# Optimization experiments

Hardware: AMD Instinct MI355X
Metric: run time of the kernel (lower is better)

The kernel has to match this reference:

```python
import math
import jax, jax.numpy as jnp
import numpy as np

B, T, D_MODEL, H = 2, 2048, 1024, 16
D_HEAD = D_MODEL // H
EPS = 1e-9


def setup_inputs() -> dict:
    key = jax.random.key(0)
    ks = jax.random.split(key, 5)
    std = 1.0 / math.sqrt(D_MODEL)
    return {
        "x": jax.random.normal(ks[0], (B, T, D_MODEL), dtype=jnp.float32),
        "Wq": jax.random.normal(ks[1], (D_MODEL, D_MODEL), dtype=jnp.float32) * std,
        "Wk": jax.random.normal(ks[2], (D_MODEL, D_MODEL), dtype=jnp.float32) * std,
        "Wv": jax.random.normal(ks[3], (D_MODEL, D_MODEL), dtype=jnp.float32) * std,
        "Wo": jax.random.normal(ks[4], (D_MODEL, D_MODEL), dtype=jnp.float32) * std,
    }


def _attention(x, Wq, Wk, Wv, Wo):
    b, t, d = x.shape
    # projections (nn.Linear without bias: y = x @ W^T)
    q = (x @ Wq.T).reshape(b, t, H, D_HEAD).transpose(0, 2, 1, 3)  # (B,H,T,dh)
    k = (x @ Wk.T).reshape(b, t, H, D_HEAD).transpose(0, 2, 1, 3)
    v = (x @ Wv.T).reshape(b, t, H, D_HEAD).transpose(0, 2, 1, 3)
    scale = 1.0 / math.sqrt(D_HEAD)
    scores = jnp.einsum("bhqd,bhkd->bhqk", q, k) * scale  # (B,H,T,T)
    causal = jnp.tril(jnp.ones((t, t), dtype=bool))
    scores = jnp.where(causal[None, None], scores, -jnp.inf)
    # stable softmax with +eps in denominator (matches online-softmax accumulation)
    m = jnp.max(scores, axis=-1, keepdims=True)
    e = jnp.exp(scores - m)
    l = jnp.sum(e, axis=-1, keepdims=True)
    attn_out = jnp.einsum("bhqk,bhkd->bhqd", e, v) / (l + EPS)
    out = attn_out.transpose(0, 2, 1, 3).reshape(b, t, d)
    return out @ Wo.T


def reference(x, Wq, Wk, Wv, Wo):
    return _attention(x, Wq, Wk, Wv, Wo)
```

## Files before the change

kernel.cpp:

```cpp
#include <hip/hip_runtime.h>


typedef __attribute__((ext_vector_type(8))) short bf16x8;
typedef __attribute__((ext_vector_type(4))) short short4v;
typedef __attribute__((ext_vector_type(4))) float f32x4;

#define T_SEQ 2048
#define D_MODEL 1024
#define NHEAD 16
#define DHEAD 64

__device__ inline short f2bf(float f) {
    unsigned u = __float_as_uint(f);
    u += 0x7fffu + ((u >> 16) & 1u);
    return (short)(u >> 16);
}

__device__ inline f32x4 mfma16(bf16x8 a, bf16x8 b, f32x4 c) {
    return __builtin_amdgcn_mfma_f32_16x16x32_bf16(a, b, c, 0, 0, 0);
}

__device__ inline void gld_lds16(const short* g, short* l) {
    __builtin_amdgcn_global_load_lds(
        (const __attribute__((address_space(1))) void*)g,
        (__attribute__((address_space(3))) void*)l, 16, 0, 0);
}

__global__ __launch_bounds__(256) void cast_kernel(const float* __restrict__ s,
                                                   short* __restrict__ d, int n) {
    int i = (blockIdx.x * 256 + threadIdx.x) * 4;
    if (i >= n) return;
    float4 v = *(const float4*)(s + i);
    short4v o = { f2bf(v.x), f2bf(v.y), f2bf(v.z), f2bf(v.w) };
    *(short4v*)(d + i) = o;
}

__global__ __launch_bounds__(256) void cast4_kernel(const float* __restrict__ s0,
                                                    const float* __restrict__ s1,
                                                    const float* __restrict__ s2,
                                                    const float* __restrict__ s3,
                                                    short* __restrict__ d) {
    const float* s = (blockIdx.y == 0) ? s0 : (blockIdx.y == 1) ? s1
                   : (blockIdx.y == 2) ? s2 : s3;
    int i = (blockIdx.x * 256 + threadIdx.x) * 4;
    float4 v = *(const float4*)(s + i);
    short4v o = { f2bf(v.x), f2bf(v.y), f2bf(v.z), f2bf(v.w) };
    *(short4v*)(d + blockIdx.y * 1048576 + i) = o;
}

template <int MODE>
__global__ __launch_bounds__(256, 2) void gemm128(const short* __restrict__ A,
                                                  const short* __restrict__ B,
                                                  void* __restrict__ C0,
                                                  void* __restrict__ C1,
                                                  void* __restrict__ C2,
                                                  int M, int N, int K) {
    __shared__ short As[4096];
    __shared__ short Bs[4096];

    const int tid = threadIdx.x;
    const int wave = tid >> 6, lane = tid & 63;
    const int g = lane >> 4, ln = lane & 15;
    const int mh = wave & 1, nh = wave >> 1;
    const int m_base = blockIdx.x * 128;
    const int n_base = blockIdx.y * 128;

    const int srow = tid >> 2;
    const int sinner = (tid & 3) * 8;
    const short* Ag = A + (long)(m_base + srow) * K + sinner;
    const short* Bg = B + (long)(n_base + srow) * K + sinner;
    const long r64 = 64 * (long)K;

    f32x4 acc[4][4];
#pragma unroll
    for (int i = 0; i < 4; i++)
#pragma unroll
        for (int j = 0; j < 4; j++) acc[i][j] = (f32x4){0.f, 0.f, 0.f, 0.f};

    for (int k0 = 0; k0 < K; k0 += 32) {
        gld_lds16(Ag + k0, As + tid * 8);
        gld_lds16(Ag + r64 + k0, As + 2048 + tid * 8);
        gld_lds16(Bg + k0, Bs + tid * 8);
        gld_lds16(Bg + r64 + k0, Bs + 2048 + tid * 8);
        __syncthreads();

        bf16x8 a[4], b[4];
#pragma unroll
        for (int mf = 0; mf < 4; mf++)
            a[mf] = *(const bf16x8*)(As + (mh * 64 + mf * 16 + ln) * 32 + g * 8);
#pragma unroll
        for (int nf = 0; nf < 4; nf++)
            b[nf] = *(const bf16x8*)(Bs + (nh * 64 + nf * 16 + ln) * 32 + g * 8);
#pragma unroll
        for (int mf = 0; mf < 4; mf++)
#pragma unroll
            for (int nf = 0; nf < 4; nf++)
                acc[mf][nf] = mfma16(a[mf], b[nf], acc[mf][nf]);
        __syncthreads();
    }

    if (MODE == 2) {
#pragma unroll
        for (int mf = 0; mf < 4; mf++)
#pragma unroll
            for (int nf = 0; nf < 4; nf++)
#pragma unroll
                for (int r = 0; r < 4; r++) {
                    int row = m_base + mh * 64 + mf * 16 + g * 4 + r;
                    int col = n_base + nh * 64 + nf * 16 + ln;
                    ((float*)C0)[(long)row * N + col] = acc[mf][nf][r];
                }
    } else {
        const int mat = n_base >> 10;
        if (mat < 2) {
            short* dst = (short*)(mat == 0 ? C0 : C1);
#pragma unroll
            for (int mf = 0; mf < 4; mf++)
#pragma unroll
                for (int nf = 0; nf < 4; nf++)
#pragma unroll
                    for (int r = 0; r < 4; r++) {
                        int row = m_base + mh * 64 + mf * 16 + g * 4 + r;
                        int cc = (n_base & 1023) + nh * 64 + nf * 16 + ln;
                        int b_ = row >> 11, t = row & 2047;
                        int h = cc >> 6, d = cc & 63;
                        dst[(((long)(b_ * NHEAD + h) * T_SEQ + t) << 6) + d] =
                            f2bf(acc[mf][nf][r]);
                    }
        } else {
            short* dst = (short*)C2;
#pragma unroll
            for (int mf = 0; mf < 4; mf++)
#pragma unroll
                for (int nf = 0; nf < 4; nf++) {
                    short4v pk = { f2bf(acc[mf][nf][0]), f2bf(acc[mf][nf][1]),
                                   f2bf(acc[mf][nf][2]), f2bf(acc[mf][nf][3]) };
                    int cc = (n_base & 1023) + nh * 64 + nf * 16 + ln;
                    int row0 = m_base + mh * 64 + mf * 16 + g * 4;
                    int b_ = row0 >> 11, t = row0 & 2047;
                    *(short4v*)(&dst[((long)(b_ * 1024 + cc) << 11) + t]) = pk;
                }
        }
    }
}

__global__ __launch_bounds__(512, 4) void flash_attn(const short* __restrict__ Q,
                                                     const short* __restrict__ Kx,
                                                     const short* __restrict__ Vt,
                                                     short* __restrict__ O) {
    __shared__ short Ks[2][4096];
    __shared__ short Vs[2][4096];
    __shared__ short ldsP[8][16][72];

    const int tid = threadIdx.x;
    const int wv = tid >> 6, lane = tid & 63;
    const int g = lane >> 4, ln = lane & 15;
    const int id = blockIdx.x;
    const int qx = 15 - (id >> 5);
    const int bh = id & 31;

    const short* Kp = Kx + (long)bh * (T_SEQ * DHEAD);
    const short* Vp = Vt + (long)bh * (DHEAD * T_SEQ);

    const int sch = tid >> 8;
    const int sr = (tid >> 2) & 63;
    const int si = (tid & 3) * 8;
    const int offK = sr * 64 + sch * 32 + si;
    const long offV = (long)sr * T_SEQ + sch * 32 + si;
    const int ldst = tid * 8;

    const float sc = 0.125f * 1.44269504089f;
    const int nt = 2 * qx + 2;
    const int qrow0 = qx * 128 + wv * 16;
    const int rl = wv * 16 + g * 4;

    const short* Qp = Q + ((long)bh * T_SEQ + qrow0) * DHEAD;
    bf16x8 qf0 = *(const bf16x8*)(Qp + ln * 64 + 8 * g);
    bf16x8 qf1 = *(const bf16x8*)(Qp + ln * 64 + 32 + 8 * g);

    f32x4 o[4];
#pragma unroll
    for (int nf = 0; nf < 4; nf++) o[nf] = (f32x4){0.f, 0.f, 0.f, 0.f};
    float li[4] = {0.f, 0.f, 0.f, 0.f};

    gld_lds16(Kp + offK, &Ks[0][ldst]);
    gld_lds16(Vp + offV, &Vs[0][ldst]);

    int buf = 0;
    for (int i = 0; i < nt; i++) {
        __syncthreads();
        if (i + 1 < nt) {
            gld_lds16(Kp + (i + 1) * 4096 + offK, &Ks[buf ^ 1][ldst]);
            gld_lds16(Vp + offV + (i + 1) * 64, &Vs[buf ^ 1][ldst]);
        }

        f32x4 s[4];
#pragma unroll
        for (int j = 0; j < 4; j++) {
            bf16x8 k0 = *(const bf16x8*)(&Ks[buf][(j * 16 + ln) * 32 + 8 * g]);
            bf16x8 k1 = *(const bf16x8*)(&Ks[buf][2048 + (j * 16 + ln) * 32 + 8 * g]);
            s[j] = mfma16(qf0, k0, (f32x4){0.f, 0.f, 0.f, 0.f});
            s[j] = mfma16(qf1, k1, s[j]);
        }

        if (i >= 2 * qx) {
            const int off = (i - 2 * qx) * 64;
#pragma unroll
            for (int j = 0; j < 4; j++) {
                int kl = off + 16 * j + ln;
#pragma unroll
                for (int r = 0; r < 4; r++)
                    if (kl > rl + r) s[j][r] = -INFINITY;
            }
        }

#pragma unroll
        for (int r = 0; r < 4; r++) {
            float e0 = __builtin_amdgcn_exp2f(s[0][r] * sc);
            float e1 = __builtin_amdgcn_exp2f(s[1][r] * sc);
            float e2 = __builtin_amdgcn_exp2f(s[2][r] * sc);
            float e3 = __builtin_amdgcn_exp2f(s[3][r] * sc);
            li[r] += (e0 + e1) + (e2 + e3);
            ldsP[wv][g * 4 + r][ln] = f2bf(e0);
            ldsP[wv][g * 4 + r][16 + ln] = f2bf(e1);
            ldsP[wv][g * 4 + r][32 + ln] = f2bf(e2);
            ldsP[wv][g * 4 + r][48 + ln] = f2bf(e3);
        }

        asm volatile("s_waitcnt lgkmcnt(0)" ::: "memory");
        bf16x8 pa0 = *(const bf16x8*)(&ldsP[wv][ln][8 * g]);
        bf16x8 pa1 = *(const bf16x8*)(&ldsP[wv][ln][32 + 8 * g]);

#pragma unroll
        for (int nf = 0; nf < 4; nf++) {
            bf16x8 v0 = *(const bf16x8*)(&Vs[buf][(nf * 16 + ln) * 32 + 8 * g]);
            bf16x8 v1 = *(const bf16x8*)(&Vs[buf][2048 + (nf * 16 + ln) * 32 + 8 * g]);
            o[nf] = mfma16(pa0, v0, o[nf]);
            o[nf] = mfma16(pa1, v1, o[nf]);
        }
        buf ^= 1;
    }

#pragma unroll
    for (int r = 0; r < 4; r++) {
        float l = li[r];
        l += __shfl_xor(l, 1);
        l += __shfl_xor(l, 2);
        l += __shfl_xor(l, 4);
        l += __shfl_xor(l, 8);
        li[r] = l;
    }
    const int b = bh >> 4, h = bh & 15;
#pragma unroll
    for (int nf = 0; nf < 4; nf++) {
#pragma unroll
        for (int r = 0; r < 4; r++) {
            int rr = qrow0 + g * 4 + r;
            float v = o[nf][r] / (li[r] + 1e-9f);
            O[((long)(b * T_SEQ + rr) << 10) + h * 64 + nf * 16 + ln] = f2bf(v);
        }
    }
}

extern "C" void kernel_launch(void* const* d_in, const int* in_sizes, int n_in,
                              void* d_out, int out_size, void* d_ws, size_t ws_size,
                              hipStream_t stream) {
    const float* x  = (const float*)d_in[0];
    const float* Wq = (const float*)d_in[1];
    const float* Wk = (const float*)d_in[2];
    const float* Wv = (const float*)d_in[3];
    const float* Wo = (const float*)d_in[4];

    char* ws = (char*)d_ws;
    short* xb  = (short*)(ws + (0ull  << 20));
    short* wqb = (short*)(ws + (8ull  << 20));
    short* wob = (short*)(ws + (14ull << 20));
    short* Qb  = (short*)(ws + (16ull << 20));
    short* Kb  = (short*)(ws + (24ull << 20));
    short* Vtb = (short*)(ws + (32ull << 20));
    short* Ab  = (short*)(ws + (40ull << 20));

    cast_kernel<<<4096, 256, 0, stream>>>(x, xb, 2 * T_SEQ * D_MODEL);
    cast4_kernel<<<dim3(1024, 4), 256, 0, stream>>>(Wq, Wk, Wv, Wo, wqb);

    gemm128<3><<<dim3(32, 24), 256, 0, stream>>>(xb, wqb, Qb, Kb, Vtb,
                                                 4096, 3072, 1024);

    flash_attn<<<512, 512, 0, stream>>>(Qb, Kb, Vtb, Ab);

    gemm128<2><<<dim3(32, 8), 256, 0, stream>>>(Ab, wob, d_out, nullptr, nullptr,
                                                4096, 1024, 1024);
}
```

Baseline: 183.7 us.

## Swizzle LDS layouts, shrink attention query tiles, split output GEMM

Applies an XOR swizzle to the column chunk used by global-to-LDS loads and the matching LDS fragment reads in both GEMMs and the attention kernel, to reduce LDS bank conflicts. The attention kernel moves from 512-thread blocks over 128-query tiles to 256-thread blocks over 64-query tiles with twice as many blocks. Only the last key tile is now masked. The output projection gets a dedicated kernel with a 128x64 tile to double its grid. More, smaller blocks improve load balance across the causal triangle, at the cost of extra per-block overhead and less K/V reuse per load.

```diff
diff --git a/kernel.cpp b/kernel.cpp
--- a/kernel.cpp
+++ b/kernel.cpp
@@ -48,13 +48,12 @@
     *(short4v*)(d + blockIdx.y * 1048576 + i) = o;
 }
 
-template <int MODE>
-__global__ __launch_bounds__(256, 2) void gemm128(const short* __restrict__ A,
-                                                  const short* __restrict__ B,
-                                                  void* __restrict__ C0,
-                                                  void* __restrict__ C1,
-                                                  void* __restrict__ C2,
-                                                  int M, int N, int K) {
+__global__ __launch_bounds__(256, 2) void gemm_qkv(const short* __restrict__ A,
+                                                   const short* __restrict__ B,
+                                                   short* __restrict__ C0,
+                                                   short* __restrict__ C1,
+                                                   short* __restrict__ C2,
+                                                   int M, int N, int K) {
     __shared__ short As[4096];
     __shared__ short Bs[4096];
 
@@ -64,11 +63,12 @@
     const int mh = wave & 1, nh = wave >> 1;
     const int m_base = blockIdx.x * 128;
     const int n_base = blockIdx.y * 128;
+    const int swz8 = 8 * (g ^ ((ln >> 1) & 3));
 
     const int srow = tid >> 2;
-    const int sinner = (tid & 3) * 8;
-    const short* Ag = A + (long)(m_base + srow) * K + sinner;
-    const short* Bg = B + (long)(n_base + srow) * K + sinner;
+    const int scol = (((tid & 3) ^ ((tid >> 3) & 3))) * 8;
+    const short* Ag = A + (long)(m_base + srow) * K + scol;
+    const short* Bg = B + (long)(n_base + srow) * K + scol;
     const long r64 = 64 * (long)K;
 
     f32x4 acc[4][4];
@@ -87,10 +87,10 @@
         bf16x8 a[4], b[4];
 #pragma unroll
         for (int mf = 0; mf < 4; mf++)
-            a[mf] = *(const bf16x8*)(As + (mh * 64 + mf * 16 + ln) * 32 + g * 8);
+            a[mf] = *(const bf16x8*)(As + (mh * 64 + mf * 16 + ln) * 32 + swz8);
 #pragma unroll
         for (int nf = 0; nf < 4; nf++)
-            b[nf] = *(const bf16x8*)(Bs + (nh * 64 + nf * 16 + ln) * 32 + g * 8);
+            b[nf] = *(const bf16x8*)(Bs + (nh * 64 + nf * 16 + ln) * 32 + swz8);
 #pragma unroll
         for (int mf = 0; mf < 4; mf++)
 #pragma unroll
@@ -99,7 +99,9 @@
         __syncthreads();
     }
 
-    if (MODE == 2) {
+    const int mat = n_base >> 10;
+    if (mat < 2) {
+        short* dst = mat == 0 ? C0 : C1;
 #pragma unroll
         for (int mf = 0; mf < 4; mf++)
 #pragma unroll
@@ -107,71 +109,116 @@
 #pragma unroll
                 for (int r = 0; r < 4; r++) {
                     int row = m_base + mh * 64 + mf * 16 + g * 4 + r;
-                    int col = n_base + nh * 64 + nf * 16 + ln;
-                    ((float*)C0)[(long)row * N + col] = acc[mf][nf][r];
+                    int cc = (n_base & 1023) + nh * 64 + nf * 16 + ln;
+                    int b_ = row >> 11, t = row & 2047;
+                    int h = cc >> 6, d = cc & 63;
+                    dst[(((long)(b_ * NHEAD + h) * T_SEQ + t) << 6) + d] =
+                        f2bf(acc[mf][nf][r]);
                 }
     } else {
-        const int mat = n_base >> 10;
-        if (mat < 2) {
-            short* dst = (short*)(mat == 0 ? C0 : C1);
-#pragma unroll
-            for (int mf = 0; mf < 4; mf++)
-#pragma unroll
-                for (int nf = 0; nf < 4; nf++)
-#pragma unroll
-                    for (int r = 0; r < 4; r++) {
-                        int row = m_base + mh * 64 + mf * 16 + g * 4 + r;
-                        int cc = (n_base & 1023) + nh * 64 + nf * 16 + ln;
-                        int b_ = row >> 11, t = row & 2047;
-                        int h = cc >> 6, d = cc & 63;
-                        dst[(((long)(b_ * NHEAD + h) * T_SEQ + t) << 6) + d] =
-                            f2bf(acc[mf][nf][r]);
-                    }
-        } else {
-            short* dst = (short*)C2;
-#pragma unroll
-            for (int mf = 0; mf < 4; mf++)
-#pragma unroll
-                for (int nf = 0; nf < 4; nf++) {
-                    short4v pk = { f2bf(acc[mf][nf][0]), f2bf(acc[mf][nf][1]),
-                                   f2bf(acc[mf][nf][2]), f2bf(acc[mf][nf][3]) };
-                    int cc = (n_base & 1023) + nh * 64 + nf * 16 + ln;
-                    int row0 = m_base + mh * 64 + mf * 16 + g * 4;
-                    int b_ = row0 >> 11, t = row0 & 2047;
-                    *(short4v*)(&dst[((long)(b_ * 1024 + cc) << 11) + t]) = pk;
-                }
-        }
-    }
-}
-
-__global__ __launch_bounds__(512, 4) void flash_attn(const short* __restrict__ Q,
-                                                     const short* __restrict__ Kx,
-                                                     const short* __restrict__ Vt,
-                                                     short* __restrict__ O) {
+        short* dst = C2;
+#pragma unroll
+        for (int mf = 0; mf < 4; mf++)
+#pragma unroll
+            for (int nf = 0; nf < 4; nf++) {
+                short4v pk = { f2bf(acc[mf][nf][0]), f2bf(acc[mf][nf][1]),
+                               f2bf(acc[mf][nf][2]), f2bf(acc[mf][nf][3]) };
+                int cc = (n_base & 1023) + nh * 64 + nf * 16 + ln;
+                int row0 = m_base + mh * 64 + mf * 16 + g * 4;
+                int b_ = row0 >> 11, t = row0 & 2047;
+                *(short4v*)(&dst[((long)(b_ * 1024 + cc) << 11) + t]) = pk;
+            }
+    }
+}
+
+__global__ __launch_bounds__(256, 2) void gemm_out(const short* __restrict__ A,
+                                                   const short* __restrict__ B,
+                                                   float* __restrict__ C,
+                                                   int M, int N, int K) {
+    __shared__ short As[4096];
+    __shared__ short Bs[2048];
+
+    const int tid = threadIdx.x;
+    const int wave = tid >> 6, lane = tid & 63;
+    const int g = lane >> 4, ln = lane & 15;
+    const int mh = wave & 1, nh = wave >> 1;
+    const int m_base = blockIdx.x * 128;
+    const int n_base = blockIdx.y * 64;
+    const int swz8 = 8 * (g ^ ((ln >> 1) & 3));
+
+    const int srow = tid >> 2;
+    const int scol = (((tid & 3) ^ ((tid >> 3) & 3))) * 8;
+    const short* Ag = A + (long)(m_base + srow) * K + scol;
+    const short* Bg = B + (long)(n_base + srow) * K + scol;
+    const long r64 = 64 * (long)K;
+
+    f32x4 acc[4][2];
+#pragma unroll
+    for (int i = 0; i < 4; i++)
+#pragma unroll
+        for (int j = 0; j < 2; j++) acc[i][j] = (f32x4){0.f, 0.f, 0.f, 0.f};
+
+    for (int k0 = 0; k0 < K; k0 += 32) {
+        gld_lds16(Ag + k0, As + tid * 8);
+        gld_lds16(Ag + r64 + k0, As + 2048 + tid * 8);
+        gld_lds16(Bg + k0, Bs + tid * 8);
+        __syncthreads();
+
+        bf16x8 a[4], b[2];
+#pragma unroll
+        for (int mf = 0; mf < 4; mf++)
+            a[mf] = *(const bf16x8*)(As + (mh * 64 + mf * 16 + ln) * 32 + swz8);
+#pragma unroll
+        for (int nf = 0; nf < 2; nf++)
+            b[nf] = *(const bf16x8*)(Bs + (nh * 32 + nf * 16 + ln) * 32 + swz8);
+#pragma unroll
+        for (int mf = 0; mf < 4; mf++)
+#pragma unroll
+            for (int nf = 0; nf < 2; nf++)
+                acc[mf][nf] = mfma16(a[mf], b[nf], acc[mf][nf]);
+        __syncthreads();
+    }
+
+#pragma unroll
+    for (int mf = 0; mf < 4; mf++)
+#pragma unroll
+        for (int nf = 0; nf < 2; nf++)
+#pragma unroll
+            for (int r = 0; r < 4; r++) {
+                int row = m_base + mh * 64 + mf * 16 + g * 4 + r;
+                int col = n_base + nh * 32 + nf * 16 + ln;
+                C[(long)row * N + col] = acc[mf][nf][r];
+            }
+}
+
+__global__ __launch_bounds__(256) void flash_attn(const short* __restrict__ Q,
+                                                  const short* __restrict__ Kx,
+                                                  const short* __restrict__ Vt,
+                                                  short* __restrict__ O) {
     __shared__ short Ks[2][4096];
     __shared__ short Vs[2][4096];
-    __shared__ short ldsP[8][16][72];
+    __shared__ short ldsP[4][16][72];
 
     const int tid = threadIdx.x;
     const int wv = tid >> 6, lane = tid & 63;
     const int g = lane >> 4, ln = lane & 15;
     const int id = blockIdx.x;
-    const int qx = 15 - (id >> 5);
+    const int qx = 31 - (id >> 5);
     const int bh = id & 31;
+    const int swz8 = 8 * (g ^ ((ln >> 1) & 3));
 
     const short* Kp = Kx + (long)bh * (T_SEQ * DHEAD);
     const short* Vp = Vt + (long)bh * (DHEAD * T_SEQ);
 
-    const int sch = tid >> 8;
-    const int sr = (tid >> 2) & 63;
-    const int si = (tid & 3) * 8;
-    const int offK = sr * 64 + sch * 32 + si;
-    const long offV = (long)sr * T_SEQ + sch * 32 + si;
+    const int sr = tid >> 2;
+    const int sc8 = (((tid & 3) ^ ((tid >> 3) & 3))) * 8;
+    const int offK0 = sr * 64 + sc8;
+    const long offV0 = (long)sr * T_SEQ + sc8;
     const int ldst = tid * 8;
 
     const float sc = 0.125f * 1.44269504089f;
-    const int nt = 2 * qx + 2;
-    const int qrow0 = qx * 128 + wv * 16;
+    const int nt = qx + 1;
+    const int qrow0 = qx * 64 + wv * 16;
     const int rl = wv * 16 + g * 4;
 
     const short* Qp = Q + ((long)bh * T_SEQ + qrow0) * DHEAD;
@@ -183,31 +230,36 @@
     for (int nf = 0; nf < 4; nf++) o[nf] = (f32x4){0.f, 0.f, 0.f, 0.f};
     float li[4] = {0.f, 0.f, 0.f, 0.f};
 
-    gld_lds16(Kp + offK, &Ks[0][ldst]);
-    gld_lds16(Vp + offV, &Vs[0][ldst]);
+    gld_lds16(Kp + offK0, &Ks[0][ldst]);
+    gld_lds16(Kp + offK0 + 32, &Ks[0][2048 + ldst]);
+    gld_lds16(Vp + offV0, &Vs[0][ldst]);
+    gld_lds16(Vp + offV0 + 32, &Vs[0][2048 + ldst]);
 
     int buf = 0;
     for (int i = 0; i < nt; i++) {
         __syncthreads();
         if (i + 1 < nt) {
-            gld_lds16(Kp + (i + 1) * 4096 + offK, &Ks[buf ^ 1][ldst]);
-            gld_lds16(Vp + offV + (i + 1) * 64, &Vs[buf ^ 1][ldst]);
+            const int kO = (i + 1) * 4096 + offK0;
+            const long vO = offV0 + (i + 1) * 64;
+            gld_lds16(Kp + kO, &Ks[buf ^ 1][ldst]);
+            gld_lds16(Kp + kO + 32, &Ks[buf ^ 1][2048 + ldst]);
+            gld_lds16(Vp + vO, &Vs[buf ^ 1][ldst]);
+            gld_lds16(Vp + vO + 32, &Vs[buf ^ 1][2048 + ldst]);
         }
 
         f32x4 s[4];
 #pragma unroll
         for (int j = 0; j < 4; j++) {
-            bf16x8 k0 = *(const bf16x8*)(&Ks[buf][(j * 16 + ln) * 32 + 8 * g]);
-            bf16x8 k1 = *(const bf16x8*)(&Ks[buf][2048 + (j * 16 + ln) * 32 + 8 * g]);
+            bf16x8 k0 = *(const bf16x8*)(&Ks[buf][(j * 16 + ln) * 32 + swz8]);
+            bf16x8 k1 = *(const bf16x8*)(&Ks[buf][2048 + (j * 16 + ln) * 32 + swz8]);
             s[j] = mfma16(qf0, k0, (f32x4){0.f, 0.f, 0.f, 0.f});
             s[j] = mfma16(qf1, k1, s[j]);
         }
 
-        if (i >= 2 * qx) {
-            const int off = (i - 2 * qx) * 64;
+        if (i == nt - 1) {
 #pragma unroll
             for (int j = 0; j < 4; j++) {
-                int kl = off + 16 * j + ln;
+                int kl = 16 * j + ln;
 #pragma unroll
                 for (int r = 0; r < 4; r++)
                     if (kl > rl + r) s[j][r] = -INFINITY;
@@ -233,8 +285,8 @@
 
 #pragma unroll
         for (int nf = 0; nf < 4; nf++) {
-            bf16x8 v0 = *(const bf16x8*)(&Vs[buf][(nf * 16 + ln) * 32 + 8 * g]);
-            bf16x8 v1 = *(const bf16x8*)(&Vs[buf][2048 + (nf * 16 + ln) * 32 + 8 * g]);
+            bf16x8 v0 = *(const bf16x8*)(&Vs[buf][(nf * 16 + ln) * 32 + swz8]);
+            bf16x8 v1 = *(const bf16x8*)(&Vs[buf][2048 + (nf * 16 + ln) * 32 + swz8]);
             o[nf] = mfma16(pa0, v0, o[nf]);
             o[nf] = mfma16(pa1, v1, o[nf]);
         }
@@ -283,11 +335,11 @@
     cast_kernel<<<4096, 256, 0, stream>>>(x, xb, 2 * T_SEQ * D_MODEL);
     cast4_kernel<<<dim3(1024, 4), 256, 0, stream>>>(Wq, Wk, Wv, Wo, wqb);
 
-    gemm128<3><<<dim3(32, 24), 256, 0, stream>>>(xb, wqb, Qb, Kb, Vtb,
-                                                 4096, 3072, 1024);
-
-    flash_attn<<<512, 512, 0, stream>>>(Qb, Kb, Vtb, Ab);
-
-    gemm128<2><<<dim3(32, 8), 256, 0, stream>>>(Ab, wob, d_out, nullptr, nullptr,
-                                                4096, 1024, 1024);
-}
+    gemm_qkv<<<dim3(32, 24), 256, 0, stream>>>(xb, wqb, Qb, Kb, Vtb,
+                                               4096, 3072, 1024);
+
+    flash_attn<<<1024, 256, 0, stream>>>(Qb, Kb, Vtb, Ab);
+
+    gemm_out<<<dim3(32, 16), 256, 0, stream>>>(Ab, wob, (float*)d_out,
+                                               4096, 1024, 1024);
+}
```

Measured after the change: 175.3 us. 1.05x faster.
